# Optimization experiments

Hardware: AMD Instinct MI355X
Metric: run time of the kernel (lower is better)

The kernel has to match this reference:

```python
import jax, jax.numpy as jnp
import numpy as np

N, E, IN_D, H, OUT_D = 50000, 800000, 128, 64, 64


def setup_inputs() -> dict:
    key = jax.random.key(0)
    ks = jax.random.split(key, 16)
    s = lambda k, shape: jax.random.normal(k, shape, dtype=jnp.float32) * (1.0 / np.sqrt(shape[0]))
    return {
        "x": jax.random.normal(ks[0], (N, IN_D), dtype=jnp.float32),
        "edge_index": jax.random.randint(ks[1], (2, E), 0, N, dtype=jnp.int32),
        "W1": s(ks[2], (IN_D, H)), "b1": jnp.zeros((H,), jnp.float32),
        "W2": s(ks[3], (H, 2 * H)), "b2": jnp.zeros((2 * H,), jnp.float32),
        "W3": s(ks[4], (2 * H, 4 * H)), "b3": jnp.zeros((4 * H,), jnp.float32),
        "dec1_w": s(ks[5], (4 * H, 2 * H, 2)), "dec1_b": jnp.zeros((2 * H,), jnp.float32),
        "dec2_w": s(ks[6], (2 * H, H, 2)), "dec2_b": jnp.zeros((H,), jnp.float32),
        "dec3_w": s(ks[7], (H, H, 2)), "dec3_b": jnp.zeros((H,), jnp.float32),
        "skip1_w": s(ks[8], (2 * H, 2 * H)), "skip1_b": jnp.zeros((2 * H,), jnp.float32),
        "skip2_w": s(ks[9], (H, H)), "skip2_b": jnp.zeros((H,), jnp.float32),
        "fin_w": s(ks[10], (OUT_D, 8 * H)), "fin_b": jnp.zeros((OUT_D,), jnp.float32),
    }


def _deconv2(x, w, b):
    # ConvTranspose1d(kernel=2, stride=2): [n,c,l] x [c,o,2] -> [n,o,2l]
    y = jnp.einsum('ncl,cok->nolk', x, w)
    n, o = x.shape[0], w.shape[1]
    return y.reshape(n, o, -1) + b[None, :, None]


def reference(x, edge_index, W1, b1, W2, b2, W3, b3, dec1_w, dec1_b, dec2_w, dec2_b,
              dec3_w, dec3_b, skip1_w, skip1_b, skip2_w, skip2_b, fin_w, fin_b):
    n = x.shape[0]
    loop = jnp.arange(n, dtype=edge_index.dtype)
    src = jnp.concatenate([edge_index[0], loop])
    tgt = jnp.concatenate([edge_index[1], loop])
    deg = jax.ops.segment_sum(jnp.ones_like(src, dtype=x.dtype), tgt, num_segments=n)
    dinv = jax.lax.rsqrt(deg)  # deg >= 1 due to self-loops
    norm = dinv[src] * dinv[tgt]  # [E+N]

    def gcn(h, W, b):
        hw = h @ W
        agg = jax.ops.segment_sum(hw[src] * norm[:, None], tgt, num_segments=n)
        return agg + b

    x1 = jax.nn.gelu(gcn(x, W1, b1))    # [N, H]
    x2 = jax.nn.gelu(gcn(x1, W2, b2))   # [N, 2H]
    x3 = jax.nn.gelu(gcn(x2, W3, b3))   # [N, 4H]

    d = _deconv2(x3[:, :, None], dec1_w, dec1_b)           # [N, 2H, 2]
    d = d + (x2 @ skip1_w.T + skip1_b)[:, :, None]
    d = _deconv2(d, dec2_w, dec2_b)                        # [N, H, 4]
    d = d + (x1 @ skip2_w.T + skip2_b)[:, :, None]
    d = _deconv2(d, dec3_w, dec3_b)                        # [N, H, 8]
    out = d.reshape(n, -1) @ fin_w.T + fin_b               # [N, OUT_D]
    return out
```

## Files before the change

### kernel.cpp

```cpp
#include <hip/hip_runtime.h>
#include <hip/hip_bf16.h>

typedef __attribute__((ext_vector_type(8))) short short8_t;
typedef __attribute__((ext_vector_type(4))) float f32x4;

#define CAP 64

__device__ __forceinline__ float gelu_f(float x) {
    float x3 = x * x * x;
    return 0.5f * x * (1.0f + tanhf(0.7978845608028654f * (x + 0.044715f * x3)));
}
__device__ __forceinline__ float b2f(unsigned short u) {
    union { float f; unsigned int i; } c; c.i = ((unsigned int)u) << 16; return c.f;
}
__device__ __forceinline__ unsigned short f2bu(float f) {
    union { float f; unsigned int i; } c; c.f = f;
    unsigned int r = c.i + 0x7fffu + ((c.i >> 16) & 1u);
    return (unsigned short)(r >> 16);
}


__device__ __forceinline__ void d_EF(int bid, int t, const float* __restrict__ dec3_w,
                                     const float* __restrict__ fin_w, float* __restrict__ EF) {
    int i2 = bid * 4 + (t >> 6), od = t & 63;
    int c3 = i2 >> 2, pp = i2 & 3;
    const float* d3 = dec3_w + c3 * 128;
    const float* fw = fin_w + od * 512;
    float s = 0.f;
    #pragma unroll
    for (int o3 = 0; o3 < 64; ++o3) {
        s += d3[o3 * 2 + 0] * fw[o3 * 8 + pp * 2 + 0];
        s += d3[o3 * 2 + 1] * fw[o3 * 8 + pp * 2 + 1];
    }
    EF[i2 * 64 + od] = s;
}

__device__ __forceinline__ void d_CEF(int bid, int t, const float* __restrict__ dec2_w,
                                      const float* __restrict__ EF, float* __restrict__ CEF) {
    int i1 = bid * 4 + (t >> 6), od = t & 63;
    int c2 = i1 >> 1, lp = i1 & 1;
    const float* d2 = dec2_w + c2 * 128;
    float s = 0.f;
    #pragma unroll
    for (int o2 = 0; o2 < 64; ++o2) {
        s += d2[o2 * 2 + 0] * EF[(o2 * 4 + lp * 2 + 0) * 64 + od];
        s += d2[o2 * 2 + 1] * EF[(o2 * 4 + lp * 2 + 1) * 64 + od];
    }
    CEF[i1 * 64 + od] = s;
}

__device__ __forceinline__ void d_comp(int sb, int od,
                       const float* __restrict__ dec1_w, const float* __restrict__ skip1_w,
                       const float* __restrict__ skip2_w,
                       const float* __restrict__ dec1_b, const float* __restrict__ skip1_b,
                       const float* __restrict__ dec2_b, const float* __restrict__ skip2_b,
                       const float* __restrict__ dec3_b, const float* __restrict__ fin_w,
                       const float* __restrict__ fin_b,
                       const float* __restrict__ CEF, const float* __restrict__ EF,
                       unsigned short* __restrict__ McatT, float* __restrict__ m0) {
    if (sb < 256) {
        const float* d1 = dec1_w + sb * 256;
        float s = 0.f;
        for (int j = 0; j < 256; ++j) s += d1[j] * CEF[j * 64 + od];
        McatT[od * 448 + sb] = f2bu(s);
    } else if (sb < 384) {
        int c = sb - 256;
        float s = 0.f;
        for (int j = 0; j < 256; ++j) s += skip1_w[(j >> 1) * 128 + c] * CEF[j * 64 + od];
        McatT[od * 448 + sb] = f2bu(s);
    } else if (sb < 448) {
        int c = sb - 384;
        float s = 0.f;
        for (int j = 0; j < 256; ++j) s += skip2_w[(j >> 2) * 64 + c] * EF[j * 64 + od];
        McatT[od * 448 + sb] = f2bu(s);
    } else {
        float s = fin_b[od];
        for (int j = 0; j < 256; ++j) s += (dec1_b[j >> 1] + skip1_b[j >> 1]) * CEF[j * 64 + od];
        for (int j = 0; j < 256; ++j) s += (dec2_b[j >> 2] + skip2_b[j >> 2]) * EF[j * 64 + od];
        for (int j = 0; j < 512; ++j) s += dec3_b[j >> 3] * fin_w[od * 512 + j];
        m0[od] = s;
    }
}

__device__ __forceinline__ void d_wconv(int bid, int t,
                        const float* __restrict__ W1, const float* __restrict__ W2,
                        const float* __restrict__ W3,
                        unsigned short* __restrict__ W1T, unsigned short* __restrict__ W2T,
                        unsigned short* __restrict__ W3T) {
    int i = bid * 256 + t;
    if (i < 8192) {
        int k = i >> 6, n = i & 63;
        W1T[n * 128 + k] = f2bu(W1[i]);
    } else if (i < 16384) {
        int j = i - 8192; int k = j >> 7, n = j & 127;
        W2T[n * 64 + k] = f2bu(W2[j]);
    } else if (i < 49152) {
        int j = i - 16384; int k = j >> 8, n = j & 255;
        W3T[n * 128 + k] = f2bu(W3[j]);
    }
}

__device__ __forceinline__ void d_fillx(int bid, int t, const int* __restrict__ src,
                                        const int* __restrict__ tgt, int E,
                                        int* __restrict__ cnt, unsigned short* __restrict__ csru) {
    int i = (bid * 256 + t) * 8;
    if (i + 7 < E) {
        int4 t0 = *(const int4*)(tgt + i);
        int4 t1 = *(const int4*)(tgt + i + 4);
        int4 s0 = *(const int4*)(src + i);
        int4 s1 = *(const int4*)(src + i + 4);
        int k0 = atomicAdd(&cnt[t0.x], 1);
        int k1 = atomicAdd(&cnt[t0.y], 1);
        int k2 = atomicAdd(&cnt[t0.z], 1);
        int k3 = atomicAdd(&cnt[t0.w], 1);
        int k4 = atomicAdd(&cnt[t1.x], 1);
        int k5 = atomicAdd(&cnt[t1.y], 1);
        int k6 = atomicAdd(&cnt[t1.z], 1);
        int k7 = atomicAdd(&cnt[t1.w], 1);
        if (k0 < CAP - 1) csru[(t0.x << 6) + k0] = (unsigned short)s0.x;
        if (k1 < CAP - 1) csru[(t0.y << 6) + k1] = (unsigned short)s0.y;
        if (k2 < CAP - 1) csru[(t0.z << 6) + k2] = (unsigned short)s0.z;
        if (k3 < CAP - 1) csru[(t0.w << 6) + k3] = (unsigned short)s0.w;
        if (k4 < CAP - 1) csru[(t1.x << 6) + k4] = (unsigned short)s1.x;
        if (k5 < CAP - 1) csru[(t1.y << 6) + k5] = (unsigned short)s1.y;
        if (k6 < CAP - 1) csru[(t1.z << 6) + k6] = (unsigned short)s1.z;
        if (k7 < CAP - 1) csru[(t1.w << 6) + k7] = (unsigned short)s1.w;
    } else {
        for (int k = i; k < E; ++k) {
            int tt = tgt[k];
            int kk = atomicAdd(&cnt[tt], 1);
            if (kk < CAP - 1) csru[(tt << 6) + kk] = (unsigned short)src[k];
        }
    }
}

template<bool A32, bool BIAS, bool GELU, bool OUT32>
__device__ __forceinline__ void d_gmm(
    int bx, int by,
    const unsigned short* __restrict__ A, const float* __restrict__ Af, int lda,
    const unsigned short* __restrict__ Bt, int ldb,
    const float* __restrict__ bias,
    void* __restrict__ Cv, int ldc, int M, int K) {
    constexpr int LDS_R = 72;
    __shared__ unsigned short As[64 * LDS_R];
    __shared__ unsigned short Bs[64 * LDS_R];
    const int tid = threadIdx.x;
    const int r0 = bx * 64, c0 = by * 64;
    const int w = tid >> 6, lane = tid & 63;
    const int wm = (w >> 1) * 32, wn = (w & 1) * 32;
    const int fr = lane & 15, kg = lane >> 4;
    f32x4 acc[2][2];
    #pragma unroll
    for (int m = 0; m < 2; ++m)
        #pragma unroll
        for (int n = 0; n < 2; ++n) { f32x4 z = {0.f, 0.f, 0.f, 0.f}; acc[m][n] = z; }

    const int sr = tid >> 2, sc = (tid & 3) * 16;
    const bool aok = (r0 + sr) < M;
    const unsigned short* ag = A32 ? nullptr : (A + (size_t)(r0 + sr) * lda + sc);
    const float* agf = A32 ? (Af + (size_t)(r0 + sr) * lda + sc) : nullptr;
    const unsigned short* bg = Bt + (size_t)(c0 + sr) * ldb + sc;

    for (int kt = 0; kt < K; kt += 64) {
        if (aok) {
            if constexpr (A32) {
                float4 f0 = *(const float4*)(agf + kt);
                float4 f1 = *(const float4*)(agf + kt + 4);
                float4 f2 = *(const float4*)(agf + kt + 8);
                float4 f3 = *(const float4*)(agf + kt + 12);
                unsigned short o[16] = { f2bu(f0.x), f2bu(f0.y), f2bu(f0.z), f2bu(f0.w),
                                         f2bu(f1.x), f2bu(f1.y), f2bu(f1.z), f2bu(f1.w),
                                         f2bu(f2.x), f2bu(f2.y), f2bu(f2.z), f2bu(f2.w),
                                         f2bu(f3.x), f2bu(f3.y), f2bu(f3.z), f2bu(f3.w) };
                *(uint4*)&As[sr * LDS_R + sc]     = ((const uint4*)o)[0];
                *(uint4*)&As[sr * LDS_R + sc + 8] = ((const uint4*)o)[1];
            } else {
                *(uint4*)&As[sr * LDS_R + sc]     = *(const uint4*)(ag + kt);
                *(uint4*)&As[sr * LDS_R + sc + 8] = *(const uint4*)(ag + kt + 8);
            }
        }
        *(uint4*)&Bs[sr * LDS_R + sc]     = *(const uint4*)(bg + kt);
        *(uint4*)&Bs[sr * LDS_R + sc + 8] = *(const uint4*)(bg + kt + 8);
        __syncthreads();
        #pragma unroll
        for (int s2 = 0; s2 < 2; ++s2) {
            short8_t afr[2], bfr[2];
            #pragma unroll
            for (int n = 0; n < 2; ++n)
                bfr[n] = *(const short8_t*)&Bs[(wn + n * 16 + fr) * LDS_R + s2 * 32 + kg * 8];
            #pragma unroll
            for (int m = 0; m < 2; ++m)
                afr[m] = *(const short8_t*)&As[(wm + m * 16 + fr) * LDS_R + s2 * 32 + kg * 8];
            #pragma unroll
            for (int m = 0; m < 2; ++m)
                #pragma unroll
                for (int n = 0; n < 2; ++n)
                    acc[m][n] = __builtin_amdgcn_mfma_f32_16x16x32_bf16(afr[m], bfr[n], acc[m][n], 0, 0, 0);
        }
        __syncthreads();
    }
    #pragma unroll
    for (int m = 0; m < 2; ++m) {
        #pragma unroll
        for (int n = 0; n < 2; ++n) {
            #pragma unroll
            for (int j = 0; j < 4; ++j) {
                int row = r0 + wm + m * 16 + kg * 4 + j;
                int col = c0 + wn + n * 16 + fr;
                if (row < M) {
                    float xv = acc[m][n][j];
                    if (BIAS) xv += bias[col];
                    if (GELU) xv = gelu_f(xv);
                    if (OUT32) ((float*)Cv)[(size_t)row * ldc + col] = xv;
                    else ((unsigned short*)Cv)[(size_t)row * ldc + col] = f2bu(xv);
                }
            }
        }
    }
}

template<int F, int LPN, int NN, bool FIRST, bool EPI>
__device__ __forceinline__ void d_aggb(
    int bid,
    const unsigned short* __restrict__ g, int ldi,
    const int* __restrict__ cnt, const unsigned short* __restrict__ csru,
    unsigned int* __restrict__ csrw,
    const float* __restrict__ bias,
    unsigned short* __restrict__ out, int ldo, int N) {
    constexpr int SLOTS = 64 / LPN;
    constexpr int NB = 24 / SLOTS;
    static_assert(F / LPN == 8, "V must be 8");
    __shared__ int   sIdx[4][NN][CAP];
    __shared__ float sW[4][NN][CAP];
    int tid = threadIdx.x;
    int lane = tid & 63, wv = tid >> 6;
    int vb = bid * (4 * NN) + wv * NN;
    int slot = lane / LPN, fl = lane % LPN;
    int fo = fl * 8;
    bool ok[NN];
    int vc[NN], degc[NN];
    #pragma unroll
    for (int n = 0; n < NN; ++n) {
        int v = vb + n;
        ok[n] = v < N;
        vc[n] = ok[n] ? v : 0;
    }
    #pragma unroll
    for (int n = 0; n < NN; ++n) {
        int ua; float ww;
        if constexpr (FIRST) {
            int deg = cnt[vc[n]];
            degc[n] = min(deg, CAP - 2);
            float dv = rsqrtf((float)(deg + 1));
            if (lane < degc[n])       { ua = csru[(vc[n] << 6) + lane]; ww = rsqrtf((float)(cnt[ua] + 1)) * dv; }
            else if (lane == degc[n]) { ua = vc[n]; ww = dv * dv; }
            else if (lane == 63)      { ua = degc[n]; ww = 0.f; }
            else                      { ua = vc[n]; ww = 0.f; }
            if (ok[n]) csrw[(vc[n] << 6) + lane] = ((unsigned int)f2bu(ww) << 16) | (unsigned int)ua;
        } else {
            unsigned int pa = csrw[(vc[n] << 6) + lane];
            ua = (int)(pa & 0xFFFFu);
            ww = b2f((unsigned short)(pa >> 16));
            degc[n] = (int)(csrw[(vc[n] << 6) + 63] & 0xFFFFu);
        }
        sIdx[wv][n][lane] = ua;
        sW[wv][n][lane] = ww;
    }
    int cmax = 0;
    #pragma unroll
    for (int n = 0; n < NN; ++n) cmax = max(cmax, ok[n] ? degc[n] + 1 : 0);
    float acc[NN][8] = {};
    const unsigned short* hbase = g + fo;

    uint4 tt[NN][NB];
    float wg[NN][NB];
    #pragma unroll
    for (int b = 0; b < NB; ++b) {
        int j = slot + b * SLOTS;
        #pragma unroll
        for (int n = 0; n < NN; ++n) {
            int u = sIdx[wv][n][j];
            wg[n][b] = sW[wv][n][j];
            tt[n][b] = *(const uint4*)(hbase + (size_t)u * ldi);
        }
    }
    #pragma unroll
    for (int b = 0; b < NB; ++b)
        #pragma unroll
        for (int n = 0; n < NN; ++n) {
            const unsigned short* pp = (const unsigned short*)&tt[n][b];
            #pragma unroll
            for (int q = 0; q < 8; ++q)
                acc[n][q] = fmaf(b2f(pp[q]), wg[n][b], acc[n][q]);
        }
    for (int j = NB * SLOTS + slot; j < cmax; j += SLOTS) {
        #pragma unroll
        for (int n = 0; n < NN; ++n) {
            int u = sIdx[wv][n][j];
            float w = sW[wv][n][j];
            uint4 t = *(const uint4*)(hbase + (size_t)u * ldi);
            const unsigned short* pp = (const unsigned short*)&t;
            #pragma unroll
            for (int q = 0; q < 8; ++q)
                acc[n][q] = fmaf(b2f(pp[q]), w, acc[n][q]);
        }
    }
    #pragma unroll
    for (int off = LPN; off < 64; off <<= 1)
        #pragma unroll
        for (int n = 0; n < NN; ++n)
            #pragma unroll
            for (int q = 0; q < 8; ++q)
                acc[n][q] += __shfl_xor(acc[n][q], off, 64);
    if (slot == 0) {
        #pragma unroll
        for (int n = 0; n < NN; ++n) {
            unsigned short o[8];
            #pragma unroll
            for (int q = 0; q < 8; ++q) {
                float xv = acc[n][q];
                if (EPI) xv = gelu_f(xv + bias[fo + q]);
                o[q] = f2bu(xv);
            }
            if (ok[n]) *(uint4*)(out + (size_t)(vb + n) * ldo + fo) = *(const uint4*)o;
        }
    }
}


template<bool A32, bool BIAS, bool GELU, bool OUT32>
__global__ __launch_bounds__(256) void k_gmm(
    const unsigned short* __restrict__ A, const float* __restrict__ Af, int lda,
    const unsigned short* __restrict__ Bt, int ldb,
    const float* __restrict__ bias,
    void* __restrict__ Cv, int ldc, int M, int K) {
    d_gmm<A32, BIAS, GELU, OUT32>(blockIdx.x, blockIdx.y, A, Af, lda, Bt, ldb, bias,
                                  Cv, ldc, M, K);
}

template<int F, int LPN, int NN, bool EPI>
__global__ __launch_bounds__(256) void k_aggb(
    const unsigned short* __restrict__ g, int ldi,
    unsigned int* __restrict__ csrw,
    const float* __restrict__ bias,
    unsigned short* __restrict__ out, int ldo, int N) {
    d_aggb<F, LPN, NN, false, EPI>(blockIdx.x, g, ldi, nullptr, nullptr, csrw, bias, out, ldo, N);
}

__global__ __launch_bounds__(256) void k_mega0(
    const float* __restrict__ W1, const float* __restrict__ W2, const float* __restrict__ W3,
    unsigned short* __restrict__ W1T, unsigned short* __restrict__ W2T,
    unsigned short* __restrict__ W3T,
    const float* __restrict__ dec3_w, const float* __restrict__ fin_w, float* __restrict__ EF,
    int* __restrict__ cnt, int N) {
    int b = blockIdx.x, t = threadIdx.x;
    if (b < 192) d_wconv(b, t, W1, W2, W3, W1T, W2T, W3T);
    else if (b < 256) d_EF(b - 192, t, dec3_w, fin_w, EF);
    else { int i = (b - 256) * 256 + t; if (i < N) cnt[i] = 0; }
}

__global__ __launch_bounds__(256) void k_megaA(
    const int* __restrict__ src, const int* __restrict__ tgt, int E,
    int* __restrict__ cnt, unsigned short* __restrict__ csru, int nf,
    const float* __restrict__ x, const unsigned short* __restrict__ W1T,
    unsigned short* __restrict__ hw1, int M, int ng,
    const float* __restrict__ dec2_w, const float* __restrict__ EF, float* __restrict__ CEF) {
    int b = blockIdx.x;
    if (b < nf)
        d_fillx(b, threadIdx.x, src, tgt, E, cnt, csru);
    else if (b < nf + ng)
        d_gmm<true, false, false, false>(b - nf, 0, nullptr, x, 128, W1T, 128,
                                         (const float*)nullptr, hw1, 64, M, 128);
    else
        d_CEF(b - nf - ng, threadIdx.x, dec2_w, EF, CEF);
}

__global__ __launch_bounds__(256) void k_megaB(
    const unsigned short* __restrict__ hw1,
    const int* __restrict__ cnt, const unsigned short* __restrict__ csru,
    unsigned int* __restrict__ csrw,
    const float* __restrict__ b1, unsigned short* __restrict__ x1out, int N, int na,
    const float* __restrict__ dec1_w, const float* __restrict__ skip1_w,
    const float* __restrict__ skip2_w,
    const float* __restrict__ dec1_b, const float* __restrict__ skip1_b,
    const float* __restrict__ dec2_b, const float* __restrict__ skip2_b,
    const float* __restrict__ dec3_b, const float* __restrict__ fin_w,
    const float* __restrict__ fin_b,
    const float* __restrict__ CEF, const float* __restrict__ EF,
    unsigned short* __restrict__ McatT, float* __restrict__ m0) {
    int b = blockIdx.x, t = threadIdx.x;
    if (b < na) {
        d_aggb<64, 8, 4, true, true>(b, hw1, 64, cnt, csru, csrw, b1, x1out, 448, N);
    } else {
        int sb = (b - na) * 4 + (t >> 6);
        if (sb <= 448)
            d_comp(sb, t & 63, dec1_w, skip1_w, skip2_w, dec1_b, skip1_b, dec2_b, skip2_b,
                   dec3_b, fin_w, fin_b, CEF, EF, McatT, m0);
    }
}

extern "C" void kernel_launch(void* const* d_in, const int* in_sizes, int n_in,
                              void* d_out, int out_size, void* d_ws, size_t ws_size,
                              hipStream_t stream) {
    const float* x       = (const float*)d_in[0];
    const int*   ei      = (const int*)d_in[1];
    const float* W1      = (const float*)d_in[2];
    const float* b1      = (const float*)d_in[3];
    const float* W2      = (const float*)d_in[4];
    const float* b2      = (const float*)d_in[5];
    const float* W3      = (const float*)d_in[6];
    const float* b3      = (const float*)d_in[7];
    const float* dec1_w  = (const float*)d_in[8];
    const float* dec1_b  = (const float*)d_in[9];
    const float* dec2_w  = (const float*)d_in[10];
    const float* dec2_b  = (const float*)d_in[11];
    const float* dec3_w  = (const float*)d_in[12];
    const float* dec3_b  = (const float*)d_in[13];
    const float* skip1_w = (const float*)d_in[14];
    const float* skip1_b = (const float*)d_in[15];
    const float* skip2_w = (const float*)d_in[16];
    const float* skip2_b = (const float*)d_in[17];
    const float* fin_w   = (const float*)d_in[18];
    const float* fin_b   = (const float*)d_in[19];

    const int N = in_sizes[0] / 128;
    const int E = in_sizes[1] / 2;
    const int* e_src = ei;
    const int* e_tgt = ei + E;

    char* p = (char*)d_ws;
    auto alloc = [&](size_t bytes) -> void* {
        void* r = p;
        p += (bytes + 255) & ~(size_t)255;
        return r;
    };
    int*            cnt   = (int*)alloc((size_t)N * 4);
    unsigned short* csru  = (unsigned short*)alloc((size_t)N * CAP * 2);
    unsigned int*   csrw  = (unsigned int*)alloc((size_t)N * CAP * 4);
    float* EF      = (float*)alloc(256 * 64 * 4);
    float* CEF     = (float*)alloc(256 * 64 * 4);
    float* m0      = (float*)alloc(64 * 4);
    unsigned short* McatT = (unsigned short*)alloc(64 * 448 * 2);
    unsigned short* W1T   = (unsigned short*)alloc(64 * 128 * 2);
    unsigned short* W2T   = (unsigned short*)alloc(128 * 64 * 2);
    unsigned short* W3T   = (unsigned short*)alloc(256 * 128 * 2);
    unsigned short* hw1   = (unsigned short*)alloc((size_t)N * 64 * 2);
    unsigned short* a1    = (unsigned short*)alloc((size_t)N * 64 * 2);
    unsigned short* xcat  = (unsigned short*)alloc((size_t)N * 448 * 2);
    unsigned short* a2    = hw1;
    if ((size_t)(p - (char*)d_ws) > ws_size) return;

    const int nf = (E / 8 + 255) / 256;
    const int mg = (N + 63) / 64;
    const int ag4 = (N + 15) / 16;
    const int ag2 = (N + 7) / 8;
    const int compb = (449 + 3) / 4;
    const int zb = (N + 255) / 256;

    k_mega0<<<dim3(192 + 64 + zb), dim3(256), 0, stream>>>(
        W1, W2, W3, W1T, W2T, W3T, dec3_w, fin_w, EF, cnt, N);

    k_megaA<<<dim3(nf + mg + 64), dim3(256), 0, stream>>>(
        e_src, e_tgt, E, cnt, csru, nf, x, W1T, hw1, N, mg, dec2_w, EF, CEF);

    k_megaB<<<dim3(ag4 + compb), dim3(256), 0, stream>>>(
        hw1, cnt, csru, csrw, b1, xcat + 384, N, ag4,
        dec1_w, skip1_w, skip2_w, dec1_b, skip1_b, dec2_b, skip2_b, dec3_b,
        fin_w, fin_b, CEF, EF, McatT, m0);

    k_aggb<64, 8, 4, false><<<dim3(ag4), dim3(256), 0, stream>>>(
        xcat + 384, 448, csrw, (const float*)nullptr, a1, 64, N);
    k_gmm<false, true, true, false><<<dim3(mg, 2), dim3(256), 0, stream>>>(
        a1, nullptr, 64, W2T, 64, b2, xcat + 256, 448, N, 64);

    k_aggb<128, 16, 2, false><<<dim3(ag2), dim3(256), 0, stream>>>(
        xcat + 256, 448, csrw, (const float*)nullptr, a2, 128, N);
    k_gmm<false, true, true, false><<<dim3(mg, 4), dim3(256), 0, stream>>>(
        a2, nullptr, 128, W3T, 128, b3, xcat, 448, N, 128);

    k_gmm<false, true, false, true><<<dim3(mg, 1), dim3(256), 0, stream>>>(
        xcat, nullptr, 448, McatT, 448, m0, d_out, 64, N, 448);
}
```

Measured before the change: 202.7 us.

## Use exp-based GELU, paired bf16 unpack, and fewer nodes per wave in 64-wide aggregation

GELU's tanh form is rewritten as x times a sigmoid computed with exp2f, which is cheaper than tanhf. The bf16-to-float unpack now handles two values per 32-bit word using a shift and a mask instead of eight separate 16-bit extractions. The 64-wide aggregation passes drop the nodes handled per wave from 4 to 2, doubling the grid to add parallelism and lower register pressure, at the cost of more blocks and less index-load amortization.

```diff
diff --git a/kernel.cpp b/kernel.cpp
--- a/kernel.cpp
+++ b/kernel.cpp
@@ -8,7 +8,8 @@
 
 __device__ __forceinline__ float gelu_f(float x) {
     float x3 = x * x * x;
-    return 0.5f * x * (1.0f + tanhf(0.7978845608028654f * (x + 0.044715f * x3)));
+    float z = 0.7978845608028654f * (x + 0.044715f * x3);
+    return x / (1.0f + exp2f(-2.8853900817779268f * z));
 }
 __device__ __forceinline__ float b2f(unsigned short u) {
     union { float f; unsigned int i; } c; c.i = ((unsigned int)u) << 16; return c.f;
@@ -17,6 +18,12 @@
     union { float f; unsigned int i; } c; c.f = f;
     unsigned int r = c.i + 0x7fffu + ((c.i >> 16) & 1u);
     return (unsigned short)(r >> 16);
+}
+__device__ __forceinline__ void b2f2(unsigned int u, float& lo, float& hi) {
+    union { float f; unsigned int i; } a, b;
+    a.i = u << 16;
+    b.i = u & 0xFFFF0000u;
+    lo = a.f; hi = b.f;
 }
 
 
@@ -288,10 +295,15 @@
     for (int b = 0; b < NB; ++b)
         #pragma unroll
         for (int n = 0; n < NN; ++n) {
-            const unsigned short* pp = (const unsigned short*)&tt[n][b];
-            #pragma unroll
-            for (int q = 0; q < 8; ++q)
-                acc[n][q] = fmaf(b2f(pp[q]), wg[n][b], acc[n][q]);
+            const unsigned int* pu = (const unsigned int*)&tt[n][b];
+            float w = wg[n][b];
+            #pragma unroll
+            for (int q = 0; q < 4; ++q) {
+                float lo, hi;
+                b2f2(pu[q], lo, hi);
+                acc[n][2 * q]     = fmaf(lo, w, acc[n][2 * q]);
+                acc[n][2 * q + 1] = fmaf(hi, w, acc[n][2 * q + 1]);
+            }
         }
     for (int j = NB * SLOTS + slot; j < cmax; j += SLOTS) {
         #pragma unroll
@@ -299,10 +311,14 @@
             int u = sIdx[wv][n][j];
             float w = sW[wv][n][j];
             uint4 t = *(const uint4*)(hbase + (size_t)u * ldi);
-            const unsigned short* pp = (const unsigned short*)&t;
-            #pragma unroll
-            for (int q = 0; q < 8; ++q)
-                acc[n][q] = fmaf(b2f(pp[q]), w, acc[n][q]);
+            const unsigned int* pu = (const unsigned int*)&t;
+            #pragma unroll
+            for (int q = 0; q < 4; ++q) {
+                float lo, hi;
+                b2f2(pu[q], lo, hi);
+                acc[n][2 * q]     = fmaf(lo, w, acc[n][2 * q]);
+                acc[n][2 * q + 1] = fmaf(hi, w, acc[n][2 * q + 1]);
+            }
         }
     }
     #pragma unroll
@@ -390,7 +406,7 @@
     unsigned short* __restrict__ McatT, float* __restrict__ m0) {
     int b = blockIdx.x, t = threadIdx.x;
     if (b < na) {
-        d_aggb<64, 8, 4, true, true>(b, hw1, 64, cnt, csru, csrw, b1, x1out, 448, N);
+        d_aggb<64, 8, 2, true, true>(b, hw1, 64, cnt, csru, csrw, b1, x1out, 448, N);
     } else {
         int sb = (b - na) * 4 + (t >> 6);
         if (sb <= 448)
@@ -452,7 +468,6 @@
 
     const int nf = (E / 8 + 255) / 256;
     const int mg = (N + 63) / 64;
-    const int ag4 = (N + 15) / 16;
     const int ag2 = (N + 7) / 8;
     const int compb = (449 + 3) / 4;
     const int zb = (N + 255) / 256;
@@ -463,12 +478,12 @@
     k_megaA<<<dim3(nf + mg + 64), dim3(256), 0, stream>>>(
         e_src, e_tgt, E, cnt, csru, nf, x, W1T, hw1, N, mg, dec2_w, EF, CEF);
 
-    k_megaB<<<dim3(ag4 + compb), dim3(256), 0, stream>>>(
-        hw1, cnt, csru, csrw, b1, xcat + 384, N, ag4,
+    k_megaB<<<dim3(ag2 + compb), dim3(256), 0, stream>>>(
+        hw1, cnt, csru, csrw, b1, xcat + 384, N, ag2,
         dec1_w, skip1_w, skip2_w, dec1_b, skip1_b, dec2_b, skip2_b, dec3_b,
         fin_w, fin_b, CEF, EF, McatT, m0);
 
-    k_aggb<64, 8, 4, false><<<dim3(ag4), dim3(256), 0, stream>>>(
+    k_aggb<64, 8, 2, false><<<dim3(ag2), dim3(256), 0, stream>>>(
         xcat + 384, 448, csrw, (const float*)nullptr, a1, 64, N);
     k_gmm<false, true, true, false><<<dim3(mg, 2), dim3(256), 0, stream>>>(
         a1, nullptr, 64, W2T, 64, b2, xcat + 256, 448, N, 64);
```

Result: slower. 207.5 us (+2.4%).
